# Kernel tuning notes

Measured on AMD Instinct MI355X. Metric: run time of the kernel, lower is better.

## Reference

```python
import jax, jax.numpy as jnp
import numpy as np

EMBED = 1024
HEADS = 16
HDIM = EMBED // HEADS
B, S = 4, 2048
NEG = -1e20


def setup_inputs() -> dict:
    key = jax.random.key(0)
    ks = jax.random.split(key, 9)
    query = jax.random.normal(ks[0], (B, S, EMBED), dtype=jnp.float32)
    key_t = jax.random.normal(ks[1], (B, S, EMBED), dtype=jnp.float32)
    value = jax.random.normal(ks[2], (B, S, EMBED), dtype=jnp.float32)
    mask = jax.random.randint(ks[3], (1, 1, S, S), 0, 2, dtype=jnp.int32)
    padding = jax.random.randint(ks[4], (B, 1, 1, S), 0, 2, dtype=jnp.int32)
    sc = 1.0 / np.sqrt(EMBED)
    Wq = jax.random.normal(ks[5], (EMBED, EMBED), dtype=jnp.float32) * sc
    Wk = jax.random.normal(ks[6], (EMBED, EMBED), dtype=jnp.float32) * sc
    Wv = jax.random.normal(ks[7], (EMBED, EMBED), dtype=jnp.float32) * sc
    Wo = jax.random.normal(ks[8], (EMBED, EMBED), dtype=jnp.float32) * sc
    return {"query": query, "key": key_t, "value": value, "mask": mask,
            "padding": padding, "Wq": Wq, "Wk": Wk, "Wv": Wv, "Wo": Wo}


def reference(query, key, value, mask, padding, Wq, Wk, Wv, Wo):
    b, q_len, _ = query.shape
    k_len = key.shape[1]
    # projections (nn.Linear: x @ W^T), split into heads
    qs = (query @ Wq.T).reshape(b, q_len, HEADS, HDIM)
    ks = (key @ Wk.T).reshape(b, k_len, HEADS, HDIM)
    vs = (value @ Wv.T).reshape(b, k_len, HEADS, HDIM)
    scale = EMBED ** 0.25
    qs = qs / scale
    ks = ks / scale
    # [b, h, q, k] scores
    dot = jnp.einsum('bkhd,bqhd->bhqk', ks, qs)
    dot = jnp.where(mask == 0, NEG, dot)
    dot = jnp.where(padding == 0, NEG, dot)
    attn = jax.nn.softmax(dot, axis=-1)
    alpha = jnp.einsum('bhqk,bkhd->bqhd', attn, vs)
    out = alpha.reshape(b, q_len, EMBED) @ Wo.T
    return out
```

## Files before the change

### kernel.cpp

```cpp
#include <hip/hip_runtime.h>
#include <stdint.h>

#define B_  4
#define S_  2048
#define E_  1024
#define H_  16
#define D_  64

typedef __bf16 bf16;
typedef __bf16 bf16x4 __attribute__((ext_vector_type(4)));
typedef __bf16 bf16x8 __attribute__((ext_vector_type(8)));
typedef float  f32x4 __attribute__((ext_vector_type(4)));
typedef float  f32x16 __attribute__((ext_vector_type(16)));
typedef uint32_t u32x4 __attribute__((ext_vector_type(4)));

__device__ __forceinline__ f32x4 mfma16(bf16x8 a, bf16x8 b, f32x4 c) {
  return __builtin_amdgcn_mfma_f32_16x16x32_bf16(a, b, c, 0, 0, 0);
}
__device__ __forceinline__ f32x16 mfma32(bf16x8 a, bf16x8 b, f32x16 c) {
  return __builtin_amdgcn_mfma_f32_32x32x16_bf16(a, b, c, 0, 0, 0);
}

__device__ __forceinline__ int sw(int row, int idx) { return idx ^ ((row & 7) << 3); }

__device__ __forceinline__ void gl_lds16(const void* g, void* l) {
  __builtin_amdgcn_global_load_lds(
      (const __attribute__((address_space(1))) void*)g,
      (__attribute__((address_space(3))) void*)l, 16, 0, 0);
}

__device__ __forceinline__ uint32_t cvtpk(float lo, float hi) {
  uint32_t r;
  asm("v_cvt_pk_bf16_f32 %0, %1, %2" : "=v"(r) : "v"(lo), "v"(hi));
  return r;
}
__device__ __forceinline__ void plswap(uint32_t& a, uint32_t& b) {
  asm("v_permlane32_swap_b32 %0, %1" : "+v"(a), "+v"(b));
}

__global__ void pack_mask_kernel(const int* __restrict__ mask, uint32_t* __restrict__ mbits) {
  int idx = blockIdx.x * 256 + threadIdx.x;
  int q = idx >> 6, w = idx & 63;
  const int* p = mask + q * S_ + w * 32;
  uint32_t bits = 0;
#pragma unroll
  for (int j = 0; j < 32; j += 4) {
    int4 v = *(const int4*)(p + j);
    bits |= (v.x != 0 ? 1u : 0u) << (j + 0);
    bits |= (v.y != 0 ? 1u : 0u) << (j + 1);
    bits |= (v.z != 0 ? 1u : 0u) << (j + 2);
    bits |= (v.w != 0 ? 1u : 0u) << (j + 3);
  }
  mbits[idx] = bits;
}

__global__ void pack_pad_kernel(const int* __restrict__ pad, uint32_t* __restrict__ pbits) {
  int idx = threadIdx.x;
  int b = idx >> 6, w = idx & 63;
  const int* p = pad + b * S_ + w * 32;
  uint32_t bits = 0;
#pragma unroll
  for (int j = 0; j < 32; j += 4) {
    int4 v = *(const int4*)(p + j);
    bits |= (v.x != 0 ? 1u : 0u) << (j + 0);
    bits |= (v.y != 0 ? 1u : 0u) << (j + 1);
    bits |= (v.z != 0 ? 1u : 0u) << (j + 2);
    bits |= (v.w != 0 ? 1u : 0u) << (j + 3);
  }
  pbits[idx] = bits;
}

__global__ __launch_bounds__(256)
void expand_mask(const uint32_t* __restrict__ mbits, const uint32_t* __restrict__ pbits,
                 uint2* __restrict__ mbt) {
  int idx = blockIdx.x * 256 + threadIdx.x;
  int q = idx & 2047;
  int kt = (idx >> 11) & 31;
  int b = idx >> 16;
  uint2 r;
  r.x = mbits[q * 64 + kt * 2 + 0] & pbits[b * 64 + kt * 2 + 0];
  r.y = mbits[q * 64 + kt * 2 + 1] & pbits[b * 64 + kt * 2 + 1];
  mbt[idx] = r;
}

__global__ __launch_bounds__(256)
void cvt_w(const float* __restrict__ w0, const float* __restrict__ w1,
           const float* __restrict__ w2, const float* __restrict__ w3,
           bf16* __restrict__ out, float sq, float sk) {
  int z = blockIdx.z;
  const float* src = z == 0 ? w0 : (z == 1 ? w1 : (z == 2 ? w2 : w3));
  float s = (z == 0) ? sq : ((z == 1) ? sk : 1.0f);
  size_t i = ((size_t)blockIdx.x * 256 + threadIdx.x) * 8;
  float4 a = *(const float4*)(src + i);
  float4 b = *(const float4*)(src + i + 4);
  bf16x8 o;
  o[0] = (bf16)(a.x * s); o[1] = (bf16)(a.y * s); o[2] = (bf16)(a.z * s); o[3] = (bf16)(a.w * s);
  o[4] = (bf16)(b.x * s); o[5] = (bf16)(b.y * s); o[6] = (bf16)(b.z * s); o[7] = (bf16)(b.w * s);
  *(bf16x8*)(out + (size_t)z * (1024ull * 1024ull) + i) = o;
}

struct GA { const void* A; const bf16* W; void* O; };

template<bool A_F32, bool OUT_F32>
__global__ __launch_bounds__(256, A_F32 ? 3 : 4)
void gemm_bf(GA g0, GA g1, GA g2) {
  GA g = (blockIdx.z == 0) ? g0 : ((blockIdx.z == 1) ? g1 : g2);
  const int id = blockIdx.x;
  const int brow = ((id & 7) * 8 + (id >> 6)) * 128;
  const int bcol = ((id >> 3) & 7) * 128;
  const int tid = threadIdx.x;
  const int l = tid & 63, wv = tid >> 6;
  const int lg = l >> 4, lr = l & 15;
  const int wr = wv >> 1, wc = wv & 1;

  __shared__ __align__(16) char smem[A_F32 ? 49152 : 32768];
  bf16* Bs = (bf16*)(smem + (A_F32 ? 32768 : 16384));

  f32x4 acc[4][4] = {};

  const int sr = l >> 3, sc8 = l & 7;
  const bf16* Bb = g.W + (size_t)(bcol + wv * 32 + sr) * E_ + (size_t)(sc8 ^ sr) * 8;
  bf16* lb = Bs + (wv * 32) * 64;

  float* Asf = (float*)smem;
  bf16*  Asb = (bf16*)smem;
  const float* AbE = nullptr; const float* AbO = nullptr;
  const bf16*  Abb = nullptr;
  const int sr4 = l >> 4, sc16 = l & 15;
  if constexpr (A_F32) {
    const float* Af = (const float*)g.A;
    AbE = Af + (size_t)(brow + wv * 32 + sr4) * E_ + (size_t)((sc16 ^ sr4) * 4);
    AbO = Af + (size_t)(brow + wv * 32 + sr4) * E_ + (size_t)((sc16 ^ (4 + sr4)) * 4);
  } else {
    Abb = (const bf16*)g.A + (size_t)(brow + wv * 32 + sr) * E_ + (size_t)(sc8 ^ sr) * 8;
  }

  for (int kt = 0; kt < E_ / 64; ++kt) {
    __syncthreads();
    if constexpr (A_F32) {
      float* la = Asf + (wv * 32) * 64;
#pragma unroll
      for (int i = 0; i < 8; ++i) {
        const float* src = ((i & 1) ? AbO : AbE) + (size_t)(i * 4) * E_ + kt * 64;
        gl_lds16(src, la + (i * 4) * 64);
      }
    } else {
      bf16* la = Asb + (wv * 32) * 64;
      const bf16* a = Abb + kt * 64;
#pragma unroll
      for (int i = 0; i < 4; ++i)
        gl_lds16(a + (size_t)i * 8 * E_, la + i * 8 * 64);
    }
    {
      const bf16* b = Bb + kt * 64;
#pragma unroll
      for (int i = 0; i < 4; ++i)
        gl_lds16(b + (size_t)i * 8 * E_, lb + i * 8 * 64);
    }
    __syncthreads();
#pragma unroll
    for (int kk = 0; kk < 2; ++kk) {
      bf16x8 af[4], bfr[4];
#pragma unroll
      for (int ms = 0; ms < 4; ++ms) {
        int row = wr * 64 + ms * 16 + lr;
        if constexpr (A_F32) {
          int g0c = 2 * (kk * 4 + lg);
          f32x4 lo  = *(const f32x4*)&Asf[row * 64 + ((g0c ^ (row & 7)) * 4)];
          f32x4 hi4 = *(const f32x4*)&Asf[row * 64 + (((g0c + 1) ^ (row & 7)) * 4)];
          u32x4 pk = { cvtpk(lo[0], lo[1]), cvtpk(lo[2], lo[3]),
                       cvtpk(hi4[0], hi4[1]), cvtpk(hi4[2], hi4[3]) };
          af[ms] = __builtin_bit_cast(bf16x8, pk);
        } else {
          af[ms] = *(const bf16x8*)&Asb[sw(row, row * 64 + kk * 32 + lg * 8)];
        }
      }
#pragma unroll
      for (int ns = 0; ns < 4; ++ns) {
        int row = wc * 64 + ns * 16 + lr;
        bfr[ns] = *(const bf16x8*)&Bs[sw(row, row * 64 + kk * 32 + lg * 8)];
      }
#pragma unroll
      for (int ms = 0; ms < 4; ++ms)
#pragma unroll
        for (int ns = 0; ns < 4; ++ns)
          acc[ms][ns] = mfma16(af[ms], bfr[ns], acc[ms][ns]);
    }
  }

  if (!OUT_F32 && blockIdx.z == 2) {
    bf16* T = (bf16*)smem;
    __syncthreads();
#pragma unroll
    for (int ms = 0; ms < 4; ++ms) {
#pragma unroll
      for (int ns = 0; ns < 4; ++ns) {
        int col = wc * 64 + ns * 16 + lr;
        int rowb = wr * 64 + ms * 16 + lg * 4;
        bf16x4 hv;
#pragma unroll
        for (int r = 0; r < 4; ++r) hv[r] = (bf16)acc[ms][ns][r];
        *(bf16x4*)&T[col * 128 + (rowb ^ ((col & 7) << 3))] = hv;
      }
    }
    __syncthreads();
    int chunk = tid & 15, dl0 = tid >> 4;
#pragma unroll
    for (int pass = 0; pass < 8; ++pass) {
      int dl = pass * 16 + dl0;
      bf16x8 v = *(const bf16x8*)&T[dl * 128 + ((chunk * 8) ^ ((dl & 7) << 3))];
      int colg = bcol + dl;
      int bh2 = (brow >> 11) * 16 + (colg >> 6);
      int d = colg & 63;
      int s0 = (brow & 2047) + chunk * 8;
      *(bf16x8*)((bf16*)g.O + ((size_t)bh2 * 64 + d) * (size_t)S_ + s0) = v;
    }
    return;
  }

#pragma unroll
  for (int ms = 0; ms < 4; ++ms) {
#pragma unroll
    for (int ns = 0; ns < 4; ++ns) {
#pragma unroll
      for (int r = 0; r < 4; ++r) {
        int row = brow + wr * 64 + ms * 16 + lg * 4 + r;
        int col = bcol + wc * 64 + ns * 16 + lr;
        if constexpr (OUT_F32) ((float*)g.O)[(size_t)row * E_ + col] = acc[ms][ns][r];
        else                   ((bf16*)g.O)[(size_t)row * E_ + col] = (bf16)acc[ms][ns][r];
      }
    }
  }
}

__global__ __launch_bounds__(256, 4)
void attn_kernel(const bf16* __restrict__ Q, const bf16* __restrict__ K,
                 const bf16* __restrict__ Vt, const uint2* __restrict__ mbt,
                 bf16* __restrict__ alpha) {
  const int raw = blockIdx.x;
  const int xcd = raw & 7, slot = raw >> 3;
  const int bh = xcd * 8 + (slot >> 4), qblk = slot & 15;
  const int b = bh >> 4, h = bh & 15;
  const int tid = threadIdx.x, wv = tid >> 6, l = tid & 63;
  const int ln = l & 31, hi = l >> 5;
  const int qw = qblk * 128 + wv * 32;
  const int sr = l >> 3, sc8 = l & 7;
  const int g = (ln & 7) ^ (ln >> 3);

  __shared__ bf16 Ks[2][64 * 64];
  __shared__ bf16 Vs[2][64 * 64];

  bf16x8 qreg[4];
#pragma unroll
  for (int dc = 0; dc < 4; ++dc)
    qreg[dc] = *(const bf16x8*)(Q + (size_t)(b * S_ + qw + ln) * E_ + h * 64 + dc * 16 + hi * 8);

  bf16x8 ones;
#pragma unroll
  for (int j = 0; j < 8; ++j) ones[j] = (bf16)1.0f;

  f32x16 o[2] = {};
  f32x16 lacc = {};

  const int c0 = (sc8 ^ sr ^ ((wv * 2) & 7)) * 8;
  const int c1 = (sc8 ^ sr ^ ((wv * 2 + 1) & 7)) * 8;
  const bf16* kp0 = K + (size_t)(b * S_ + wv * 16 + sr) * E_ + h * 64 + c0;
  const bf16* kp1 = K + (size_t)(b * S_ + wv * 16 + 8 + sr) * E_ + h * 64 + c1;
  const bf16* vp0 = Vt + ((size_t)bh * 64 + wv * 16 + sr) * S_ + c0;
  const bf16* vp1 = Vt + ((size_t)bh * 64 + wv * 16 + 8 + sr) * S_ + c1;
  const uint2* mrow = mbt + ((size_t)b << 16) + qw + ln;

  auto stage = [&](int buf) {
    gl_lds16(kp0, Ks[buf] + (wv * 16) * 64);
    gl_lds16(kp1, Ks[buf] + (wv * 16 + 8) * 64);
    gl_lds16(vp0, Vs[buf] + (wv * 16) * 64);
    gl_lds16(vp1, Vs[buf] + (wv * 16 + 8) * 64);
    kp0 += (size_t)64 * E_;
    kp1 += (size_t)64 * E_;
    vp0 += 64;
    vp1 += 64;
  };

  stage(0);
  __syncthreads();

  for (int kt = 0; kt < 32; ++kt) {
    const int cur = kt & 1;
    if (kt < 31) stage(cur ^ 1);

    f32x16 sc[2] = {};
    __builtin_amdgcn_s_setprio(1);
#pragma unroll
    for (int ct = 0; ct < 2; ++ct) {
#pragma unroll
      for (int dc = 0; dc < 4; ++dc) {
        int row = ct * 32 + ln;
        int c = (dc * 2 + hi) ^ g ^ (ct * 4);
        bf16x8 kf = *(const bf16x8*)&Ks[cur][row * 64 + c * 8];
        sc[ct] = mfma32(kf, qreg[dc], sc[ct]);
      }
    }
    __builtin_amdgcn_s_setprio(0);

    uint2 mv = *mrow;
    mrow += 2048;
    uint32_t mq[2];
    mq[0] = mv.x >> (hi * 4);
    mq[1] = mv.y >> (hi * 4);

    uint32_t up[16];
#pragma unroll
    for (int ct = 0; ct < 2; ++ct) {
      float p[16];
#pragma unroll
      for (int r = 0; r < 16; ++r) {
        const int rel = (r & 3) + 8 * (r >> 2);
        float pe = __builtin_amdgcn_exp2f(sc[ct][r]);
        uint32_t keep = (uint32_t)__builtin_amdgcn_sbfe(mq[ct], rel, 1);
        p[r] = __builtin_bit_cast(float, __builtin_bit_cast(uint32_t, pe) & keep);
      }
#pragma unroll
      for (int j = 0; j < 8; ++j)
        up[ct * 8 + j] = cvtpk(p[2 * j], p[2 * j + 1]);
    }

#pragma unroll
    for (int kc = 0; kc < 4; ++kc) {
      const int ct = kc >> 1, base = ct * 8 + (kc & 1) * 4;
      plswap(up[base + 0], up[base + 2]);
      plswap(up[base + 1], up[base + 3]);
      u32x4 w = {up[base + 0], up[base + 1], up[base + 2], up[base + 3]};
      bf16x8 pf = __builtin_bit_cast(bf16x8, w);
      __builtin_amdgcn_s_setprio(1);
#pragma unroll
      for (int dt = 0; dt < 2; ++dt) {
        int row = dt * 32 + ln;
        int c = (kc * 2 + hi) ^ g ^ (dt * 4);
        bf16x8 vf = *(const bf16x8*)&Vs[cur][row * 64 + c * 8];
        o[dt] = mfma32(vf, pf, o[dt]);
      }
      lacc = mfma32(ones, pf, lacc);
      __builtin_amdgcn_s_setprio(0);
    }
    __syncthreads();
  }

  float inv = 1.0f / lacc[0];
  size_t qoff = (size_t)(b * S_ + qw + ln) * E_ + h * 64;
#pragma unroll
  for (int dt = 0; dt < 2; ++dt) {
#pragma unroll
    for (int rg = 0; rg < 4; ++rg) {
      bf16x4 ov;
#pragma unroll
      for (int j = 0; j < 4; ++j) ov[j] = (bf16)(o[dt][rg * 4 + j] * inv);
      *(bf16x4*)(alpha + qoff + dt * 32 + rg * 8 + hi * 4) = ov;
    }
  }
}

extern "C" void kernel_launch(void* const* d_in, const int* in_sizes, int n_in,
                              void* d_out, int out_size, void* d_ws, size_t ws_size,
                              hipStream_t stream) {
  const float* query = (const float*)d_in[0];
  const float* key_t = (const float*)d_in[1];
  const float* value = (const float*)d_in[2];
  const int*   mask  = (const int*)d_in[3];
  const int*   pad   = (const int*)d_in[4];
  const float* Wq    = (const float*)d_in[5];
  const float* Wk    = (const float*)d_in[6];
  const float* Wv    = (const float*)d_in[7];
  const float* Wo    = (const float*)d_in[8];

  char* ws = (char*)d_ws;
  bf16* alpha = (bf16*)ws;
  bf16* Wb    = (bf16*)(ws + ((size_t)16 << 20));
  bf16* QKV   = (bf16*)(ws + ((size_t)24 << 20));
  uint32_t* mbits = (uint32_t*)(ws + ((size_t)72 << 20));
  uint32_t* pbits = mbits + (size_t)S_ * 64;
  uint2*    mbt   = (uint2*)(ws + ((size_t)73 << 20));

  const size_t AM = 8192ull * 1024ull;
  const size_t WM = 1024ull * 1024ull;
  bf16* Vt = QKV + 2 * AM;

  pack_mask_kernel<<<512, 256, 0, stream>>>(mask, mbits);
  pack_pad_kernel<<<1, 256, 0, stream>>>(pad, pbits);
  expand_mask<<<1024, 256, 0, stream>>>(mbits, pbits, mbt);

  const float qscale = 0.17677669529663687f;
  const float log2e  = 1.4426950408889634f;
  cvt_w<<<dim3(512, 1, 4), 256, 0, stream>>>(Wq, Wk, Wv, Wo, Wb, qscale * log2e, qscale);

  GA gq{query, Wb,          QKV};
  GA gk{key_t, Wb + WM,     QKV + AM};
  GA gv{value, Wb + 2 * WM, Vt};
  gemm_bf<true, false><<<dim3(512, 1, 3), 256, 0, stream>>>(gq, gk, gv);

  attn_kernel<<<1024, 256, 0, stream>>>(QKV, QKV + AM, Vt, mbt, alpha);

  GA go{alpha, Wb + 3 * WM, d_out};
  gemm_bf<false, true><<<dim3(512, 1, 1), 256, 0, stream>>>(go, go, go);
}
```

Before: 208.2 us.

## Convert fp32 A tiles to bf16 once via register prefetch before LDS store

In the fp32-input projection GEMM, A tiles were copied as fp32 into LDS and converted to bf16 by every wave at fragment-read time. Now each thread loads the next fp32 A tile into registers during the current tile's MFMA work, converts it once, and stores bf16 into a swizzled LDS buffer. This halves the A tile's LDS footprint, so the launch bound rises to 4 blocks per CU, and it removes the redundant per-read conversions. The trade-off is higher register pressure from the prefetched fp32 values, and the global loads now go through VGPRs instead of direct-to-LDS copies.

```diff
diff --git a/kernel.cpp b/kernel.cpp
--- a/kernel.cpp
+++ b/kernel.cpp
@@ -102,7 +102,7 @@
 struct GA { const void* A; const bf16* W; void* O; };
 
 template<bool A_F32, bool OUT_F32>
-__global__ __launch_bounds__(256, A_F32 ? 3 : 4)
+__global__ __launch_bounds__(256, 4)
 void gemm_bf(GA g0, GA g1, GA g2) {
   GA g = (blockIdx.z == 0) ? g0 : ((blockIdx.z == 1) ? g1 : g2);
   const int id = blockIdx.x;
@@ -112,40 +112,53 @@
   const int l = tid & 63, wv = tid >> 6;
   const int lg = l >> 4, lr = l & 15;
   const int wr = wv >> 1, wc = wv & 1;
-
-  __shared__ __align__(16) char smem[A_F32 ? 49152 : 32768];
-  bf16* Bs = (bf16*)(smem + (A_F32 ? 32768 : 16384));
+  const int sr = l >> 3, sc8 = l & 7;
+
+  __shared__ __align__(16) char smem[32768];
+  bf16* As = (bf16*)smem;
+  bf16* Bs = (bf16*)(smem + 16384);
 
   f32x4 acc[4][4] = {};
 
-  const int sr = l >> 3, sc8 = l & 7;
   const bf16* Bb = g.W + (size_t)(bcol + wv * 32 + sr) * E_ + (size_t)(sc8 ^ sr) * 8;
   bf16* lb = Bs + (wv * 32) * 64;
 
-  float* Asf = (float*)smem;
-  bf16*  Asb = (bf16*)smem;
-  const float* AbE = nullptr; const float* AbO = nullptr;
-  const bf16*  Abb = nullptr;
-  const int sr4 = l >> 4, sc16 = l & 15;
+  const bf16* Abb = nullptr;
+  const float* Ap = nullptr;
+  f32x4 a0[4], a1[4];
   if constexpr (A_F32) {
-    const float* Af = (const float*)g.A;
-    AbE = Af + (size_t)(brow + wv * 32 + sr4) * E_ + (size_t)((sc16 ^ sr4) * 4);
-    AbO = Af + (size_t)(brow + wv * 32 + sr4) * E_ + (size_t)((sc16 ^ (4 + sr4)) * 4);
+    Ap = (const float*)g.A + (size_t)(brow + wv * 32 + sr) * E_ + sc8 * 8;
   } else {
     Abb = (const bf16*)g.A + (size_t)(brow + wv * 32 + sr) * E_ + (size_t)(sc8 ^ sr) * 8;
   }
+
+  auto loadA = [&]() {
+#pragma unroll
+    for (int i = 0; i < 4; ++i) {
+      const float* p = Ap + (size_t)(8 * i) * E_;
+      a0[i] = *(const f32x4*)p;
+      a1[i] = *(const f32x4*)(p + 4);
+    }
+    Ap += 64;
+  };
+  auto writeA = [&]() {
+#pragma unroll
+    for (int i = 0; i < 4; ++i) {
+      int row = wv * 32 + sr + 8 * i;
+      u32x4 pk = { cvtpk(a0[i][0], a0[i][1]), cvtpk(a0[i][2], a0[i][3]),
+                   cvtpk(a1[i][0], a1[i][1]), cvtpk(a1[i][2], a1[i][3]) };
+      *(bf16x8*)&As[sw(row, row * 64 + sc8 * 8)] = __builtin_bit_cast(bf16x8, pk);
+    }
+  };
+
+  if constexpr (A_F32) loadA();
 
   for (int kt = 0; kt < E_ / 64; ++kt) {
     __syncthreads();
     if constexpr (A_F32) {
-      float* la = Asf + (wv * 32) * 64;
-#pragma unroll
-      for (int i = 0; i < 8; ++i) {
-        const float* src = ((i & 1) ? AbO : AbE) + (size_t)(i * 4) * E_ + kt * 64;
-        gl_lds16(src, la + (i * 4) * 64);
-      }
+      writeA();
     } else {
-      bf16* la = Asb + (wv * 32) * 64;
+      bf16* la = As + (wv * 32) * 64;
       const bf16* a = Abb + kt * 64;
 #pragma unroll
       for (int i = 0; i < 4; ++i)
@@ -158,22 +171,16 @@
         gl_lds16(b + (size_t)i * 8 * E_, lb + i * 8 * 64);
     }
     __syncthreads();
+    if constexpr (A_F32) {
+      if (kt + 1 < E_ / 64) loadA();
+    }
 #pragma unroll
     for (int kk = 0; kk < 2; ++kk) {
       bf16x8 af[4], bfr[4];
 #pragma unroll
       for (int ms = 0; ms < 4; ++ms) {
         int row = wr * 64 + ms * 16 + lr;
-        if constexpr (A_F32) {
-          int g0c = 2 * (kk * 4 + lg);
-          f32x4 lo  = *(const f32x4*)&Asf[row * 64 + ((g0c ^ (row & 7)) * 4)];
-          f32x4 hi4 = *(const f32x4*)&Asf[row * 64 + (((g0c + 1) ^ (row & 7)) * 4)];
-          u32x4 pk = { cvtpk(lo[0], lo[1]), cvtpk(lo[2], lo[3]),
-                       cvtpk(hi4[0], hi4[1]), cvtpk(hi4[2], hi4[3]) };
-          af[ms] = __builtin_bit_cast(bf16x8, pk);
-        } else {
-          af[ms] = *(const bf16x8*)&Asb[sw(row, row * 64 + kk * 32 + lg * 8)];
-        }
+        af[ms] = *(const bf16x8*)&As[sw(row, row * 64 + kk * 32 + lg * 8)];
       }
 #pragma unroll
       for (int ns = 0; ns < 4; ++ns) {
```

New measurement: 210.1 us, median of 2. Within noise of the previous version (+0.9%).
